# Kernel tuning notes

Measured on AMD Instinct MI355X. Metric: run time of the kernel, lower is better.

## Reference

```python
import jax, jax.numpy as jnp
import numpy as np
from jax import lax

A = 20            # len(ANCHOR_RATIOS)=4 * len(ANCHOR_SCALES)=5 in neural-motifs config
TGT = 6           # anchor_target_dim
DIM = 512
IN_DIM = 1024
B, H, W = 16, 37, 37


def setup_inputs() -> dict:
    key = jax.random.key(0)
    k1, k2, k3, k4, k5 = jax.random.split(key, 5)
    fmap = jax.random.normal(k1, (B, IN_DIM, H, W), dtype=jnp.float32)
    # conv weights in OIHW, fan-in scaled init
    W1 = jax.random.normal(k2, (DIM, IN_DIM, 3, 3), dtype=jnp.float32) / np.sqrt(IN_DIM * 9)
    b1 = jnp.zeros((DIM,), dtype=jnp.float32)
    W2 = jax.random.normal(k3, (TGT * A, DIM, 1, 1), dtype=jnp.float32) / np.sqrt(DIM)
    b2 = jnp.zeros((TGT * A,), dtype=jnp.float32)
    return {"fmap": fmap, "W1": W1, "b1": b1, "W2": W2, "b2": b2}


def reference(fmap, W1, b1, W2, b2):
    dn = ("NCHW", "OIHW", "NCHW")
    # 3x3 conv, padding=1
    x = lax.conv_general_dilated(fmap, W1, window_strides=(1, 1), padding="SAME",
                                 dimension_numbers=dn) + b1[None, :, None, None]
    # ReLU6
    x = jnp.clip(x, 0.0, 6.0)
    # 1x1 conv -> [B, 6*A, H, W]
    x = lax.conv_general_dilated(x, W2, window_strides=(1, 1), padding="VALID",
                                 dimension_numbers=dn) + b2[None, :, None, None]
    # _reshape_channels: [B, C, H, W] -> [B, H, W, C], then split C -> (A, 6)
    b, c, h, w = x.shape
    x = jnp.transpose(x, (0, 2, 3, 1))
    return x.reshape(b, h, w, A, TGT)
```

## Files before the change

kernel.cpp:

```cpp
#include <hip/hip_runtime.h>
#include <stdint.h>

#define HW   1369
#define QW   39
#define QP   1616
#define QT   1536
#define CIN  1024
#define CMID 512
#define KTOT 9216
#define NTIL 144
#define ASL  12288
#define BBASE 36864
#define BSL  16384

typedef float  f32x4  __attribute__((ext_vector_type(4)));
typedef __bf16 bf16x8 __attribute__((ext_vector_type(8)));

__device__ __forceinline__ uint16_t f2bf(float f) {
  uint32_t u = __float_as_uint(f);
  u += 0x7fffu + ((u >> 16) & 1u);
  return (uint16_t)(u >> 16);
}

__device__ __forceinline__ void gll16(const void* g, void* l) {
  const __attribute__((address_space(1))) uint32_t* ga =
      (const __attribute__((address_space(1))) uint32_t*)(uintptr_t)g;
  __attribute__((address_space(3))) uint32_t* la =
      (__attribute__((address_space(3))) uint32_t*)(uint32_t)(uintptr_t)l;
  __builtin_amdgcn_global_load_lds(ga, la, 16, 0, 0);
}

__global__ void k_pad_transpose(const float* __restrict__ fmap, uint16_t* __restrict__ Xp) {
  __shared__ float t[32][33];
  const int b = blockIdx.z;
  const int c0 = blockIdx.y * 32;
  const int p0 = blockIdx.x * 32;
  const int tx = threadIdx.x, ty = threadIdx.y;
  const float* src = fmap + ((size_t)b * CIN + c0) * HW + p0;
#pragma unroll
  for (int i = 0; i < 4; ++i) {
    int cc = ty + i * 8;
    t[cc][tx] = (p0 + tx < HW) ? src[(size_t)cc * HW + tx] : 0.f;
  }
  __syncthreads();
#pragma unroll
  for (int i = 0; i < 4; ++i) {
    int pl = ty + i * 8;
    int p = p0 + pl;
    if (p < HW) {
      int h = p / 37, w = p - h * 37;
      int q = (h + 1) * QW + (w + 1);
      Xp[((size_t)b * QP + q) * CIN + c0 + tx] = f2bf(t[tx][pl]);
    }
  }
}

__global__ void k_pack_w1(const float* __restrict__ W1, uint16_t* __restrict__ Apk) {
  int idx = blockIdx.x * 256 + threadIdx.x;
  if (idx >= 512 * KTOT) return;
  int o = idx / KTOT, k = idx - o * KTOT;
  int r = k >> 10, c = k & 1023;
  Apk[idx] = f2bf(W1[((size_t)o * CIN + c) * 9 + r]);
}

__global__ void k_pack_w2(const float* __restrict__ W2, uint16_t* __restrict__ W2p) {
  int idx = blockIdx.x * 256 + threadIdx.x;
  int j = idx >> 9, o = idx & 511;
  W2p[idx] = (j < 120) ? f2bf(W2[j * 512 + o]) : (uint16_t)0;
}

__global__ __launch_bounds__(512, 1) void k_conv1(
    const uint16_t* __restrict__ Xp, const uint16_t* __restrict__ Apk,
    const float* __restrict__ b1, uint16_t* __restrict__ x1) {
  __shared__ __align__(16) uint16_t lds[BBASE + 2 * BSL];

  const int tid  = threadIdx.x;
  const int wid  = tid >> 6, lane = tid & 63;
  const int lrow = lane & 15, lq = lane >> 4;
  const int wm   = wid >> 2,  wn = wid & 3;

  const int bid = blockIdx.x;
  const int g   = (bid & 7) * 32 + (bid >> 3);
  const int mt  = g >> 1, nt = g & 1;
  const int batch = mt >> 3, qb = (mt & 7) * 192;
  const int o0 = nt * 256;
  const uint16_t* Xb = Xp + (size_t)batch * QP * CIN;

  const int xorb    = (lrow & 7) << 4;
  const int col_el0 = ((lq * 16) ^ xorb) >> 1;
  const int col_el1 = col_el0 ^ 32;

  const int scol = ((tid & 7) ^ ((tid >> 3) & 7)) * 8;
  const int srow = tid >> 3;

  f32x4 acc[6][4] = {};

#define STAGEA(u) do {                                                                \
    if ((u) < NTIL) {                                                                 \
      const int cb_  = (u) / 9;                                                       \
      const int tap_ = (u) - cb_ * 9;                                                 \
      const int off_ = (tap_ / 3) * QW + tap_ % 3;                                    \
      const int c0_  = cb_ << 6;                                                      \
      uint16_t* sl = lds + ((u) % 3) * ASL;                                           \
      _Pragma("unroll")                                                               \
      for (int j = 0; j < 3; ++j)                                                     \
        gll16(Xb + (size_t)(qb + off_ + j * 64 + srow) * CIN + c0_ + scol,            \
              sl + j * 4096 + wid * 512);                                             \
    }                                                                                 \
  } while (0)

#define STAGEB(u) do {                                                                \
    if ((u) < NTIL) {                                                                 \
      const int cb_  = (u) / 9;                                                       \
      const int tap_ = (u) - cb_ * 9;                                                 \
      const int c0_  = cb_ << 6;                                                      \
      uint16_t* sl = lds + BBASE + ((u) & 1) * BSL;                                   \
      _Pragma("unroll")                                                               \
      for (int j = 0; j < 4; ++j)                                                     \
        gll16(Apk + (size_t)(o0 + j * 64 + srow) * KTOT + (tap_ << 10) + c0_ + scol,  \
              sl + j * 4096 + wid * 512);                                             \
    }                                                                                 \
  } while (0)

  STAGEB(0);
  STAGEA(0);
  STAGEA(1);

  for (int t = 0; t < NTIL; ++t) {
    const uint16_t* As = lds + (t % 3) * ASL;
    const uint16_t* Bs = lds + BBASE + (t & 1) * BSL;
    if (t == NTIL - 1) asm volatile("s_waitcnt vmcnt(0)" ::: "memory");
    else               asm volatile("s_waitcnt vmcnt(3)" ::: "memory");
    asm volatile("s_barrier" ::: "memory");
    __builtin_amdgcn_sched_barrier(0);
    STAGEB(t + 1);
    STAGEA(t + 2);

    bf16x8 av0[6], av1[6], bv0[4], bv1[4];
#pragma unroll
    for (int n = 0; n < 4; ++n) {
      const uint16_t* br = Bs + (wn * 64 + n * 16 + lrow) * 64;
      bv0[n] = *(const bf16x8*)(br + col_el0);
      bv1[n] = *(const bf16x8*)(br + col_el1);
    }
#pragma unroll
    for (int m = 0; m < 6; ++m) {
      const uint16_t* ar = As + (wm * 96 + m * 16 + lrow) * 64;
      av0[m] = *(const bf16x8*)(ar + col_el0);
      av1[m] = *(const bf16x8*)(ar + col_el1);
    }
    __builtin_amdgcn_s_setprio(1);
#pragma unroll
    for (int m = 0; m < 6; ++m)
#pragma unroll
      for (int n = 0; n < 4; ++n)
        acc[m][n] = __builtin_amdgcn_mfma_f32_16x16x32_bf16(av0[m], bv0[n], acc[m][n], 0, 0, 0);
#pragma unroll
    for (int m = 0; m < 6; ++m)
#pragma unroll
      for (int n = 0; n < 4; ++n)
        acc[m][n] = __builtin_amdgcn_mfma_f32_16x16x32_bf16(av1[m], bv1[n], acc[m][n], 0, 0, 0);
    __builtin_amdgcn_s_setprio(0);
  }

  const int qr = lq * 4;
#pragma unroll
  for (int n = 0; n < 4; ++n) {
    const int o = o0 + wn * 64 + n * 16 + lrow;
    const float bias = b1[o];
#pragma unroll
    for (int m = 0; m < 6; ++m) {
#pragma unroll
      for (int v = 0; v < 4; ++v) {
        const int q = qb + wm * 96 + m * 16 + qr + v;
        float x = acc[m][n][v] + bias;
        x = fminf(fmaxf(x, 0.f), 6.f);
        x1[((size_t)batch * QT + q) * CMID + o] = f2bf(x);
      }
    }
  }
#undef STAGEB
#undef STAGEA
}

__global__ __launch_bounds__(256, 2) void k_conv2(
    const uint16_t* __restrict__ x1, const uint16_t* __restrict__ W2p,
    const float* __restrict__ b2, float* __restrict__ out) {
  __shared__ __align__(16) uint16_t lA[128 * 64];
  __shared__ __align__(16) uint16_t lB[128 * 64];
  const int tid = threadIdx.x;
  const int wid = tid >> 6, lane = tid & 63;
  const int b = blockIdx.z, q0 = blockIdx.x * 128;
  const uint16_t* Ab = x1 + (size_t)b * QT * CMID;
  const int wm = wid >> 1, wn = wid & 1;
  const int lrow = lane & 15, lk = (lane >> 4) * 8;
  f32x4 acc[4][4] = {};

  for (int kt = 0; kt < 8; ++kt) {
    const int c0 = kt << 6;
#pragma unroll
    for (int i = 0; i < 4; ++i) {
      int wb = i * 256 + wid * 64;
      int chunk = wb + lane;
      int row = chunk >> 3, ch = chunk & 7;
      gll16(Ab + (size_t)(q0 + row) * CMID + c0 + ch * 8, lA + wb * 8);
      gll16(W2p + (size_t)row * CMID + c0 + ch * 8, lB + wb * 8);
    }
    __syncthreads();
#pragma unroll
    for (int kk = 0; kk < 2; ++kk) {
      bf16x8 av[4], bv[4];
#pragma unroll
      for (int mi = 0; mi < 4; ++mi)
        av[mi] = *(const bf16x8*)(lA + (wm * 64 + mi * 16 + lrow) * 64 + kk * 32 + lk);
#pragma unroll
      for (int ni = 0; ni < 4; ++ni)
        bv[ni] = *(const bf16x8*)(lB + (wn * 64 + ni * 16 + lrow) * 64 + kk * 32 + lk);
#pragma unroll
      for (int mi = 0; mi < 4; ++mi)
#pragma unroll
        for (int ni = 0; ni < 4; ++ni)
          acc[mi][ni] = __builtin_amdgcn_mfma_f32_16x16x32_bf16(av[mi], bv[ni], acc[mi][ni], 0, 0, 0);
    }
    __syncthreads();
  }

  const int qr = (lane >> 4) * 4;
#pragma unroll
  for (int ni = 0; ni < 4; ++ni) {
    int j = wn * 64 + ni * 16 + lrow;
    if (j < 120) {
      float bias = b2[j];
#pragma unroll
      for (int mi = 0; mi < 4; ++mi) {
#pragma unroll
        for (int v = 0; v < 4; ++v) {
          int q = q0 + wm * 64 + mi * 16 + qr + v;
          int h = q / QW, w = q - h * QW;
          if (h < 37 && w < 37) {
            out[((size_t)b * HW + h * 37 + w) * 120 + j] = acc[mi][ni][v] + bias;
          }
        }
      }
    }
  }
}

extern "C" void kernel_launch(void* const* d_in, const int* in_sizes, int n_in,
                              void* d_out, int out_size, void* d_ws, size_t ws_size,
                              hipStream_t stream) {
  const float* fmap = (const float*)d_in[0];
  const float* W1   = (const float*)d_in[1];
  const float* b1   = (const float*)d_in[2];
  const float* W2   = (const float*)d_in[3];
  const float* b2   = (const float*)d_in[4];
  float* out = (float*)d_out;

  uint8_t* ws = (uint8_t*)d_ws;
  const size_t XP_BYTES  = (size_t)16 * QP * CIN * 2;
  const size_t W1P_BYTES = (size_t)512 * KTOT * 2;
  const size_t W2P_BYTES = (size_t)128 * 512 * 2;
  uint16_t* Xp  = (uint16_t*)ws;
  uint16_t* Apk = (uint16_t*)(ws + XP_BYTES);
  uint16_t* W2p = (uint16_t*)(ws + XP_BYTES + W1P_BYTES);
  uint16_t* x1  = (uint16_t*)(ws + XP_BYTES + W1P_BYTES + W2P_BYTES);

  hipMemsetAsync(Xp, 0, XP_BYTES, stream);
  k_pad_transpose<<<dim3(43, 32, 16), dim3(32, 8), 0, stream>>>(fmap, Xp);
  k_pack_w1<<<dim3((512 * KTOT + 255) / 256), dim3(256), 0, stream>>>(W1, Apk);
  k_pack_w2<<<dim3(256), dim3(256), 0, stream>>>(W2, W2p);
  k_conv1<<<dim3(256), dim3(512), 0, stream>>>(Xp, Apk, b1, x1);
  k_conv2<<<dim3(12, 1, 16), dim3(256), 0, stream>>>(x1, W2p, b2, out);
}
```

Before: 263.3 us.

## Software-pipeline LDS fragment reads across k-tiles in the conv1 GEMM main loop

The conv1 main loop is restructured into a ping-pong window scheme. Each window reads both k-halves of the A/B fragments from LDS using inline ds_read_b128 with precomputed byte offsets. The second-half MFMAs are deferred to the next window, where they overlap the new tile's LDS reads. Manual lgkmcnt waits and sched_barriers enforce ordering. The aim is to hide LDS read latency behind MFMA work, at the cost of an extra register set of fragments and reliance on the LDS array sitting at address zero.

```diff
diff --git a/kernel.cpp b/kernel.cpp
--- a/kernel.cpp
+++ b/kernel.cpp
@@ -88,12 +88,22 @@
 
   const int xorb    = (lrow & 7) << 4;
   const int col_el0 = ((lq * 16) ^ xorb) >> 1;
-  const int col_el1 = col_el0 ^ 32;
+
+  int a_off[6], b_off[4];
+#pragma unroll
+  for (int m = 0; m < 6; ++m)
+    a_off[m] = ((wm * 96 + m * 16 + lrow) * 64 + col_el0) * 2;
+#pragma unroll
+  for (int n = 0; n < 4; ++n)
+    b_off[n] = ((wn * 64 + n * 16 + lrow) * 64 + col_el0) * 2;
 
   const int scol = ((tid & 7) ^ ((tid >> 3) & 7)) * 8;
   const int srow = tid >> 3;
 
   f32x4 acc[6][4] = {};
+
+#define DSREAD(dst, abyte)                                                            \
+  asm volatile("ds_read_b128 %0, %1" : "=v"(dst) : "v"(abyte) : "memory")
 
 #define STAGEA(u) do {                                                                \
     if ((u) < NTIL) {                                                                 \
@@ -122,46 +132,55 @@
     }                                                                                 \
   } while (0)
 
+#define MFMA_SET(AV, BV) do {                                                         \
+    __builtin_amdgcn_s_setprio(1);                                                    \
+    _Pragma("unroll")                                                                 \
+    for (int m = 0; m < 6; ++m)                                                       \
+      _Pragma("unroll")                                                               \
+      for (int n = 0; n < 4; ++n)                                                     \
+        acc[m][n] = __builtin_amdgcn_mfma_f32_16x16x32_bf16(                          \
+            AV[m], BV[n], acc[m][n], 0, 0, 0);                                        \
+    __builtin_amdgcn_s_setprio(0);                                                    \
+  } while (0)
+
+#define WINDOW(T, INav, INbv, OUTav, OUTbv, FIRST, LAST) do {                         \
+    if (LAST) asm volatile("s_waitcnt vmcnt(0)" ::: "memory");                        \
+    else      asm volatile("s_waitcnt vmcnt(3)" ::: "memory");                        \
+    asm volatile("s_barrier" ::: "memory");                                           \
+    __builtin_amdgcn_sched_barrier(0);                                                \
+    const int as_b = ((T) % 3) * 24576;                                               \
+    const int bs_b = 73728 + ((T) & 1) * 32768;                                       \
+    bf16x8 av0[6], bv0[4];                                                            \
+    _Pragma("unroll")                                                                 \
+    for (int n = 0; n < 4; ++n) DSREAD(bv0[n], b_off[n] + bs_b);                      \
+    _Pragma("unroll")                                                                 \
+    for (int m = 0; m < 6; ++m) DSREAD(av0[m], a_off[m] + as_b);                      \
+    _Pragma("unroll")                                                                 \
+    for (int n = 0; n < 4; ++n) DSREAD(OUTbv[n], (b_off[n] ^ 64) + bs_b);             \
+    _Pragma("unroll")                                                                 \
+    for (int m = 0; m < 6; ++m) DSREAD(OUTav[m], (a_off[m] ^ 64) + as_b);             \
+    STAGEB((T) + 1);                                                                  \
+    STAGEA((T) + 2);                                                                  \
+    if (!(FIRST)) MFMA_SET(INav, INbv);                                               \
+    asm volatile("s_waitcnt lgkmcnt(10)" ::: "memory");                               \
+    __builtin_amdgcn_sched_barrier(0);                                                \
+    MFMA_SET(av0, bv0);                                                               \
+    asm volatile("s_waitcnt lgkmcnt(0)" ::: "memory");                                \
+    __builtin_amdgcn_sched_barrier(0);                                                \
+  } while (0)
+
   STAGEB(0);
   STAGEA(0);
   STAGEA(1);
 
-  for (int t = 0; t < NTIL; ++t) {
-    const uint16_t* As = lds + (t % 3) * ASL;
-    const uint16_t* Bs = lds + BBASE + (t & 1) * BSL;
-    if (t == NTIL - 1) asm volatile("s_waitcnt vmcnt(0)" ::: "memory");
-    else               asm volatile("s_waitcnt vmcnt(3)" ::: "memory");
-    asm volatile("s_barrier" ::: "memory");
-    __builtin_amdgcn_sched_barrier(0);
-    STAGEB(t + 1);
-    STAGEA(t + 2);
-
-    bf16x8 av0[6], av1[6], bv0[4], bv1[4];
-#pragma unroll
-    for (int n = 0; n < 4; ++n) {
-      const uint16_t* br = Bs + (wn * 64 + n * 16 + lrow) * 64;
-      bv0[n] = *(const bf16x8*)(br + col_el0);
-      bv1[n] = *(const bf16x8*)(br + col_el1);
-    }
-#pragma unroll
-    for (int m = 0; m < 6; ++m) {
-      const uint16_t* ar = As + (wm * 96 + m * 16 + lrow) * 64;
-      av0[m] = *(const bf16x8*)(ar + col_el0);
-      av1[m] = *(const bf16x8*)(ar + col_el1);
-    }
-    __builtin_amdgcn_s_setprio(1);
-#pragma unroll
-    for (int m = 0; m < 6; ++m)
-#pragma unroll
-      for (int n = 0; n < 4; ++n)
-        acc[m][n] = __builtin_amdgcn_mfma_f32_16x16x32_bf16(av0[m], bv0[n], acc[m][n], 0, 0, 0);
-#pragma unroll
-    for (int m = 0; m < 6; ++m)
-#pragma unroll
-      for (int n = 0; n < 4; ++n)
-        acc[m][n] = __builtin_amdgcn_mfma_f32_16x16x32_bf16(av1[m], bv1[n], acc[m][n], 0, 0, 0);
-    __builtin_amdgcn_s_setprio(0);
-  }
+  bf16x8 avX[6], bvX[4], avY[6], bvY[4];
+  WINDOW(0, avY, bvY, avX, bvX, 1, 0);
+  for (int t = 1; t <= NTIL - 3; t += 2) {
+    WINDOW(t,     avX, bvX, avY, bvY, 0, 0);
+    WINDOW(t + 1, avY, bvY, avX, bvX, 0, 0);
+  }
+  WINDOW(NTIL - 1, avX, bvX, avY, bvY, 0, 1);
+  MFMA_SET(avY, bvY);
 
   const int qr = lq * 4;
 #pragma unroll
@@ -179,8 +198,11 @@
       }
     }
   }
+#undef WINDOW
+#undef MFMA_SET
 #undef STAGEB
 #undef STAGEA
+#undef DSREAD
 }
 
 __global__ __launch_bounds__(256, 2) void k_conv2(
```

After: 317.4 us. +20.6%, slower.

## Shrink conv1 tiles to 192x128 with 256-thread blocks, two per CU

Applied to the files above, without the earlier changes.

The conv1 implicit GEMM tile shrinks from 192x256 outputs with 8 waves to 192x128 with 4 waves. Grid size doubles to 512 blocks and launch bounds now target two blocks per CU. The 3-stage A / 2-stage B LDS pipeline becomes a plain double buffer with a full vmcnt(0) wait each iteration. The aim is more blocks per CU so one block's waits overlap another's compute. In exchange, each A tile is loaded twice as often (less reuse), and each block's prefetch depth drops.

```diff
diff --git a/kernel.cpp b/kernel.cpp
--- a/kernel.cpp
+++ b/kernel.cpp
@@ -10,8 +10,8 @@
 #define KTOT 9216
 #define NTIL 144
 #define ASL  12288
-#define BBASE 36864
-#define BSL  16384
+#define BB   24576
+#define BSL  8192
 
 typedef float  f32x4  __attribute__((ext_vector_type(4)));
 typedef __bf16 bf16x8 __attribute__((ext_vector_type(8)));
@@ -69,21 +69,21 @@
   W2p[idx] = (j < 120) ? f2bf(W2[j * 512 + o]) : (uint16_t)0;
 }
 
-__global__ __launch_bounds__(512, 1) void k_conv1(
+__global__ __launch_bounds__(256, 2) void k_conv1(
     const uint16_t* __restrict__ Xp, const uint16_t* __restrict__ Apk,
     const float* __restrict__ b1, uint16_t* __restrict__ x1) {
-  __shared__ __align__(16) uint16_t lds[BBASE + 2 * BSL];
+  __shared__ __align__(16) uint16_t lds[2 * ASL + 2 * BSL];
 
   const int tid  = threadIdx.x;
   const int wid  = tid >> 6, lane = tid & 63;
   const int lrow = lane & 15, lq = lane >> 4;
-  const int wm   = wid >> 2,  wn = wid & 3;
+  const int wm   = wid >> 1,  wn = wid & 1;
 
   const int bid = blockIdx.x;
-  const int g   = (bid & 7) * 32 + (bid >> 3);
-  const int mt  = g >> 1, nt = g & 1;
+  const int g   = (bid & 7) * 64 + (bid >> 3);
+  const int mt  = g >> 2, nt = g & 3;
   const int batch = mt >> 3, qb = (mt & 7) * 192;
-  const int o0 = nt * 256;
+  const int o0 = nt * 128;
   const uint16_t* Xb = Xp + (size_t)batch * QP * CIN;
 
   const int xorb    = (lrow & 7) << 4;
@@ -95,46 +95,34 @@
 
   f32x4 acc[6][4] = {};
 
-#define STAGEA(u) do {                                                                \
+#define STAGE(u) do {                                                                 \
     if ((u) < NTIL) {                                                                 \
       const int cb_  = (u) / 9;                                                       \
       const int tap_ = (u) - cb_ * 9;                                                 \
       const int off_ = (tap_ / 3) * QW + tap_ % 3;                                    \
       const int c0_  = cb_ << 6;                                                      \
-      uint16_t* sl = lds + ((u) % 3) * ASL;                                           \
+      uint16_t* sa = lds + ((u) & 1) * ASL;                                           \
+      uint16_t* sb = lds + BB + ((u) & 1) * BSL;                                      \
       _Pragma("unroll")                                                               \
-      for (int j = 0; j < 3; ++j)                                                     \
-        gll16(Xb + (size_t)(qb + off_ + j * 64 + srow) * CIN + c0_ + scol,            \
-              sl + j * 4096 + wid * 512);                                             \
+      for (int j = 0; j < 6; ++j)                                                     \
+        gll16(Xb + (size_t)(qb + off_ + j * 32 + srow) * CIN + c0_ + scol,            \
+              sa + (j * 256 + wid * 64) * 8);                                         \
+      _Pragma("unroll")                                                               \
+      for (int j = 0; j < 4; ++j)                                                     \
+        gll16(Apk + (size_t)(o0 + j * 32 + srow) * KTOT + (tap_ << 10) + c0_ + scol,  \
+              sb + (j * 256 + wid * 64) * 8);                                         \
     }                                                                                 \
   } while (0)
 
-#define STAGEB(u) do {                                                                \
-    if ((u) < NTIL) {                                                                 \
-      const int cb_  = (u) / 9;                                                       \
-      const int tap_ = (u) - cb_ * 9;                                                 \
-      const int c0_  = cb_ << 6;                                                      \
-      uint16_t* sl = lds + BBASE + ((u) & 1) * BSL;                                   \
-      _Pragma("unroll")                                                               \
-      for (int j = 0; j < 4; ++j)                                                     \
-        gll16(Apk + (size_t)(o0 + j * 64 + srow) * KTOT + (tap_ << 10) + c0_ + scol,  \
-              sl + j * 4096 + wid * 512);                                             \
-    }                                                                                 \
-  } while (0)
-
-  STAGEB(0);
-  STAGEA(0);
-  STAGEA(1);
+  STAGE(0);
 
   for (int t = 0; t < NTIL; ++t) {
-    const uint16_t* As = lds + (t % 3) * ASL;
-    const uint16_t* Bs = lds + BBASE + (t & 1) * BSL;
-    if (t == NTIL - 1) asm volatile("s_waitcnt vmcnt(0)" ::: "memory");
-    else               asm volatile("s_waitcnt vmcnt(3)" ::: "memory");
+    const uint16_t* As = lds + (t & 1) * ASL;
+    const uint16_t* Bs = lds + BB + (t & 1) * BSL;
+    asm volatile("s_waitcnt vmcnt(0)" ::: "memory");
     asm volatile("s_barrier" ::: "memory");
     __builtin_amdgcn_sched_barrier(0);
-    STAGEB(t + 1);
-    STAGEA(t + 2);
+    STAGE(t + 1);
 
     bf16x8 av0[6], av1[6], bv0[4], bv1[4];
 #pragma unroll
@@ -179,8 +167,7 @@
       }
     }
   }
-#undef STAGEB
-#undef STAGEA
+#undef STAGE
 }
 
 __global__ __launch_bounds__(256, 2) void k_conv2(
@@ -269,6 +256,6 @@
   k_pad_transpose<<<dim3(43, 32, 16), dim3(32, 8), 0, stream>>>(fmap, Xp);
   k_pack_w1<<<dim3((512 * KTOT + 255) / 256), dim3(256), 0, stream>>>(W1, Apk);
   k_pack_w2<<<dim3(256), dim3(256), 0, stream>>>(W2, W2p);
-  k_conv1<<<dim3(256), dim3(512), 0, stream>>>(Xp, Apk, b1, x1);
+  k_conv1<<<dim3(512), dim3(256), 0, stream>>>(Xp, Apk, b1, x1);
   k_conv2<<<dim3(12, 1, 16), dim3(256), 0, stream>>>(x1, W2p, b2, out);
 }
```

After: 252.7 us. -4.0%, faster.
